# Kernel tuning notes

Hardware: AMD Instinct MI355X
Metric: run time of the kernel (lower is better)

The kernel has to match this reference:

```python
import jax, jax.numpy as jnp
import numpy as np

COMMITMENT_COST = 0.25


def setup_inputs() -> dict:
    key = jax.random.key(0)
    k1, k2 = jax.random.split(key)
    # z_latents: [B, H, W, D] encoder output latents
    z_latents = jax.random.normal(k1, (128, 32, 32, 64), dtype=jnp.float32)
    # embeddings: [D, K] codebook, uniform init like tf.random_uniform_initializer (default [-0.05, 0.05])
    embeddings = jax.random.uniform(k2, (64, 1024), dtype=jnp.float32, minval=-0.05, maxval=0.05)
    return {"z_latents": z_latents, "embeddings": embeddings}


def reference(z_latents, embeddings):
    d, k = embeddings.shape
    flat = z_latents.reshape(-1, d)  # [N, D]
    # squared L2 distances to each codebook entry: [N, K]
    distances = (
        jnp.sum(flat * flat, axis=1, keepdims=True)
        - 2.0 * (flat @ embeddings)
        + jnp.sum(embeddings * embeddings, axis=0, keepdims=True)
    )
    # argmax(-d) == argmin(d) (both take first occurrence on ties)
    encoding_indices = jnp.argmin(distances, axis=1)  # [N]
    # one-hot @ embeddings.T is just a gather of codebook rows
    quantized = jnp.take(embeddings.T, encoding_indices, axis=0).reshape(z_latents.shape)
    commitment_loss = jnp.mean((jax.lax.stop_gradient(quantized) - z_latents) ** 2)
    embedding_loss = jnp.mean((jax.lax.stop_gradient(z_latents) - quantized) ** 2)
    vq_loss = embedding_loss + COMMITMENT_COST * commitment_loss
    # straight-through estimator
    quantized_st = z_latents + jax.lax.stop_gradient(quantized - z_latents)
    return quantized_st, vq_loss
```

## Files before the change

kernel.cpp:

```cpp
#include <hip/hip_runtime.h>

#pragma clang fp contract(off)

typedef __attribute__((ext_vector_type(8))) short short8;
typedef __attribute__((ext_vector_type(4))) float f32x4;

#define MARGIN 0.02f

static __device__ __forceinline__ unsigned short f2b(float f) {
    union { float f; unsigned u; } x; x.f = f;
    unsigned u = x.u;
    return (unsigned short)((u + 0x7FFFu + ((u >> 16) & 1u)) >> 16);
}

template <int ES>
static __device__ __forceinline__ float np_dist(
    const float* __restrict__ zr, const float* __restrict__ ecol,
    float zn, float en) {
    float c = 0.f;
    #pragma unroll
    for (int i = 0; i < 64; ++i) c = fmaf(zr[i], ecol[i * ES], c);
    float t = zn - 2.f * c;
    return t + en;
}

template <bool ET, bool EB>
__global__ __launch_bounds__(256) void vq_prep_all(
    const float* __restrict__ E, float* __restrict__ ws_loss,
    float* __restrict__ enorm, float* __restrict__ Et,
    unsigned* __restrict__ EbW) {
    const int t = blockIdx.x * 256 + threadIdx.x;
    if (ET) {
        Et[t] = E[(t & 63) * 1024 + (t >> 6)];
    }
    if (EB) {
        if (t < 32768) {
            const int st = t >> 12;
            const int r = t & 4095;
            const int col = r >> 5;
            const int w = r & 31;
            const int g = w >> 2;
            const int d0 = ((g ^ (col & 7)) << 3) | ((w & 3) << 1);
            const int gc = st * 128 + col;
            const unsigned lo = f2b(E[d0 * 1024 + gc]);
            const unsigned hi = f2b(E[(d0 + 1) * 1024 + gc]);
            EbW[t] = lo | (hi << 16);
        }
    }
    if (t < 1024) {
        const float* colp = E + t;
        float s2 = 0.f;
        #pragma unroll
        for (int d = 0; d < 64; ++d) {
            float v = colp[d * 1024];
            s2 = fmaf(v, v, s2);
        }
        enorm[t] = s2;
        if (t == 0) *ws_loss = 0.f;
    }
}

template <bool USE_ET, bool USE_EB>
__global__ __launch_bounds__(256) void vq_main(
    const float* __restrict__ z, const float* __restrict__ E,
    const float* __restrict__ Et, const unsigned short* __restrict__ Eb,
    const float* __restrict__ enorm,
    float* __restrict__ ws_loss, float* __restrict__ out) {
    __shared__ unsigned short sB[2][128 * 64];
    __shared__ float sEn[1024];
    __shared__ float sZn[128];
    __shared__ int sIdx[128];
    __shared__ float sRed[4];

    const int tid = threadIdx.x;
    const int w = tid >> 6;
    const int l = tid & 63;
    const int quad = l >> 4;
    const int m = l & 15;
    const int b = blockIdx.x;

    ((float4*)sEn)[tid] = ((const float4*)enorm)[tid];

    if (tid < 128) {
        const float* zr = z + (b * 128 + tid) * 64;
        float S[16];
        #pragma unroll
        for (int u = 0; u < 16; ++u) { float v = zr[u]; S[u] = v * v; }
        #pragma unroll
        for (int t = 1; t < 4; ++t)
            #pragma unroll
            for (int u = 0; u < 16; ++u) {
                float v = zr[16 * t + u];
                float sq = v * v;
                S[u] = S[u] + sq;
            }
        float R0 = (S[0] + S[4]) + (S[8] + S[12]);
        float R1 = (S[1] + S[5]) + (S[9] + S[13]);
        float R2 = (S[2] + S[6]) + (S[10] + S[14]);
        float R3 = (S[3] + S[7]) + (S[11] + S[15]);
        sZn[tid] = (R0 + R1) + (R2 + R3);
    }

    short8 a[2][2];
    #pragma unroll
    for (int rt = 0; rt < 2; ++rt) {
        const int rowl = w * 32 + rt * 16 + m;
        #pragma unroll
        for (int s = 0; s < 2; ++s) {
            const float* zp = z + (b * 128 + rowl) * 64 + s * 32 + quad * 8;
            union { float4 v; float f[4]; } u0, u1;
            u0.v = *(const float4*)zp;
            u1.v = *(const float4*)(zp + 4);
            short8 av;
            #pragma unroll
            for (int j = 0; j < 4; ++j) av[j] = (short)f2b(u0.f[j]);
            #pragma unroll
            for (int j = 0; j < 4; ++j) av[4 + j] = (short)f2b(u1.f[j]);
            a[rt][s] = av;
        }
    }

    float v1p[2][4], v2p[2][4];
    #pragma unroll
    for (int rt = 0; rt < 2; ++rt)
        #pragma unroll
        for (int r = 0; r < 4; ++r) { v1p[rt][r] = 3.4e38f; v2p[rt][r] = 3.4e38f; }

    short8 nx0, nx1, nx2, nx3;
    if (USE_EB) {
        const short8* s0 = (const short8*)Eb;
        short8* dp = (short8*)sB[0];
        #pragma unroll
        for (int i = 0; i < 4; ++i) dp[tid + i * 256] = s0[tid + i * 256];
        __syncthreads();
    }

    for (int st = 0; st < 8; ++st) {
        const unsigned short* sBc;
        if (USE_EB) {
            if (st < 7) {
                const short8* sn = (const short8*)(Eb + (st + 1) * 8192);
                nx0 = sn[tid];
                nx1 = sn[tid + 256];
                nx2 = sn[tid + 512];
                nx3 = sn[tid + 768];
            }
            sBc = sB[st & 1];
        } else {
            #pragma unroll
            for (int i = 0; i < 4; ++i) {
                const int u = tid + i * 256;
                const int d0 = (u & 31) * 2;
                const int cg = u >> 5;
                const float* e0 = E + d0 * 1024 + st * 128 + cg * 4;
                union { float4 v; float f[4]; } va, vb;
                va.v = *(const float4*)e0;
                vb.v = *(const float4*)(e0 + 1024);
                #pragma unroll
                for (int j = 0; j < 4; ++j) {
                    const int col = cg * 4 + j;
                    const unsigned lo = f2b(va.f[j]);
                    const unsigned hi = f2b(vb.f[j]);
                    const int gi = col * 8 + ((d0 >> 3) ^ (col & 7));
                    *(unsigned*)&sB[0][gi * 8 + (d0 & 7)] = lo | (hi << 16);
                }
            }
            __syncthreads();
            sBc = sB[0];
        }

        #pragma unroll
        for (int ct = 0; ct < 8; ++ct) {
            const int c = st * 8 + ct;
            const int colb = (ct * 16 + m) * 8;
            short8 b0 = *(const short8*)&sBc[(colb + (quad ^ (m & 7))) * 8];
            short8 b1 = *(const short8*)&sBc[(colb + ((4 + quad) ^ (m & 7))) * 8];
            f32x4 acc0 = {0.f, 0.f, 0.f, 0.f};
            f32x4 acc1 = {0.f, 0.f, 0.f, 0.f};
            acc0 = __builtin_amdgcn_mfma_f32_16x16x32_bf16(a[0][0], b0, acc0, 0, 0, 0);
            acc0 = __builtin_amdgcn_mfma_f32_16x16x32_bf16(a[0][1], b1, acc0, 0, 0, 0);
            acc1 = __builtin_amdgcn_mfma_f32_16x16x32_bf16(a[1][0], b0, acc1, 0, 0, 0);
            acc1 = __builtin_amdgcn_mfma_f32_16x16x32_bf16(a[1][1], b1, acc1, 0, 0, 0);
            const float en = sEn[c * 16 + m];
            #pragma unroll
            for (int r = 0; r < 4; ++r) {
                float p0 = fmaf(-2.f, acc0[r], en);
                p0 = __uint_as_float((__float_as_uint(p0) & 0xFFFFFFC0u) | (unsigned)c);
                v2p[0][r] = __builtin_amdgcn_fmed3f(p0, v1p[0][r], v2p[0][r]);
                v1p[0][r] = fminf(p0, v1p[0][r]);
                float p1 = fmaf(-2.f, acc1[r], en);
                p1 = __uint_as_float((__float_as_uint(p1) & 0xFFFFFFC0u) | (unsigned)c);
                v2p[1][r] = __builtin_amdgcn_fmed3f(p1, v1p[1][r], v2p[1][r]);
                v1p[1][r] = fminf(p1, v1p[1][r]);
            }
        }

        if (USE_EB) {
            if (st < 7) {
                short8* dn = (short8*)sB[(st & 1) ^ 1];
                dn[tid] = nx0;
                dn[tid + 256] = nx1;
                dn[tid + 512] = nx2;
                dn[tid + 768] = nx3;
            }
            __syncthreads();
        } else {
            __syncthreads();
        }
    }

    float la = 0.f;
    #pragma unroll
    for (int rt = 0; rt < 2; ++rt) {
        #pragma unroll
        for (int r = 0; r < 4; ++r) {
            float pv1 = v1p[rt][r];
            float vb = pv1;
            #pragma unroll
            for (int mask = 1; mask <= 8; mask <<= 1)
                vb = fminf(vb, __shfl_xor(vb, mask));
            const int rowl = w * 32 + rt * 16 + quad * 4 + r;
            const float zn = sZn[rowl];
            const float* zr = z + (b * 128 + rowl) * 64;
            float d = 3.4e38f;
            int kk = 0x7fffffff;
            if (pv1 <= vb + MARGIN) {
                kk = (int)(__float_as_uint(pv1) & 63u) * 16 + m;
                d = USE_ET ? np_dist<1>(zr, Et + kk * 64, zn, sEn[kk])
                           : np_dist<1024>(zr, E + kk, zn, sEn[kk]);
            }
            float pv2 = v2p[rt][r];
            if (pv2 <= vb + MARGIN) {
                int kc = (int)(__float_as_uint(pv2) & 63u) * 16 + m;
                float dd = USE_ET ? np_dist<1>(zr, Et + kc * 64, zn, sEn[kc])
                                  : np_dist<1024>(zr, E + kc, zn, sEn[kc]);
                if (dd < d || (dd == d && kc < kk)) { d = dd; kk = kc; }
            }
            #pragma unroll
            for (int mask = 1; mask <= 8; mask <<= 1) {
                float d2 = __shfl_xor(d, mask);
                int c2 = __shfl_xor(kk, mask);
                bool take = (d2 < d) || (d2 == d && c2 < kk);
                d = take ? d2 : d;
                kk = take ? c2 : kk;
            }
            if (m == 0) {
                sIdx[rowl] = kk;
                la += d;
            }
        }
    }
    __syncthreads();

    {
        const int row_local = w * 32 + (l >> 1);
        const int half = l & 1;
        const int idx = sIdx[row_local];
        union { float s[32]; float4 f[8]; } tmp;
        if (USE_ET) {
            const float4* src = (const float4*)(Et + idx * 64 + half * 32);
            #pragma unroll
            for (int q4 = 0; q4 < 8; ++q4) tmp.f[q4] = src[q4];
        } else {
            #pragma unroll
            for (int dd = 0; dd < 32; ++dd) tmp.s[dd] = E[(half * 32 + dd) * 1024 + idx];
        }
        float4* dst = (float4*)(out + (b * 128 + row_local) * 64 + half * 32);
        #pragma unroll
        for (int q4 = 0; q4 < 8; ++q4) dst[q4] = tmp.f[q4];
    }

    #pragma unroll
    for (int mask = 32; mask >= 1; mask >>= 1) la += __shfl_xor(la, mask);
    if (l == 0) sRed[w] = la;
    __syncthreads();
    if (tid == 0) atomicAdd(ws_loss, sRed[0] + sRed[1] + sRed[2] + sRed[3]);
}

__global__ void vq_final(const float* __restrict__ ws_loss,
                         float* __restrict__ out) {
    out[8388608] = (*ws_loss) * (1.25f / 8388608.f);
}

extern "C" void kernel_launch(void* const* d_in, const int* in_sizes, int n_in,
                              void* d_out, int out_size, void* d_ws, size_t ws_size,
                              hipStream_t stream) {
    const float* z = (const float*)d_in[0];
    const float* E = (const float*)d_in[1];
    float* out = (float*)d_out;

    char* ws = (char*)d_ws;
    float* loss = (float*)ws;
    float* enorm = (float*)(ws + 128);
    unsigned short* Eb = (unsigned short*)(ws + 8192);
    float* Et = (float*)(ws + 139264);
    const bool useEb = ws_size >= (size_t)139264;
    const bool useEt = ws_size >= (size_t)401408;

    if (useEt) {
        vq_prep_all<true, true><<<256, 256, 0, stream>>>(E, loss, enorm, Et, (unsigned*)Eb);
        vq_main<true, true><<<1024, 256, 0, stream>>>(z, E, Et, Eb, enorm, loss, out);
    } else if (useEb) {
        vq_prep_all<false, true><<<256, 256, 0, stream>>>(E, loss, enorm, Et, (unsigned*)Eb);
        vq_main<false, true><<<1024, 256, 0, stream>>>(z, E, Et, Eb, enorm, loss, out);
    } else {
        vq_prep_all<false, false><<<256, 256, 0, stream>>>(E, loss, enorm, Et, (unsigned*)Eb);
        vq_main<false, false><<<1024, 256, 0, stream>>>(z, E, Et, Eb, enorm, loss, out);
    }
    vq_final<<<1, 1, 0, stream>>>(loss, out);
}
```

Baseline: 158.4 us.

## Read MFMA-ready codebook fragments straight from global and fuse loss finalization

The prep kernel now stages a 64-column slab of the codebook in shared memory and writes the bf16 codebook in a per-lane MFMA fragment layout. The main kernel loads B fragments straight from global/L2, dropping the double-buffered LDS staging and its per-stage barriers, which also shrinks LDS use and may allow more resident blocks. The separate finalize launch is replaced by a last-block-done atomic counter that writes the loss. This trades LDS traffic and syncs for repeated L2 reads of the 128KB codebook by every wave.

```diff
diff --git a/kernel.cpp b/kernel.cpp
--- a/kernel.cpp
+++ b/kernel.cpp
@@ -27,37 +27,54 @@
 template <bool ET, bool EB>
 __global__ __launch_bounds__(256) void vq_prep_all(
     const float* __restrict__ E, float* __restrict__ ws_loss,
-    float* __restrict__ enorm, float* __restrict__ Et,
-    unsigned* __restrict__ EbW) {
-    const int t = blockIdx.x * 256 + threadIdx.x;
+    unsigned* __restrict__ ws_cnt, float* __restrict__ enorm,
+    float* __restrict__ Et, unsigned* __restrict__ EbW) {
+    __shared__ float sT[64][65];
+    const int tid = threadIdx.x;
+    const int w = tid >> 6;
+    const int m64 = tid & 63;
+    const int c0 = blockIdx.x * 64;
+
+    #pragma unroll
+    for (int r = 0; r < 16; ++r) {
+        const int row = r * 4 + w;
+        sT[row][m64] = E[row * 1024 + c0 + m64];
+    }
+    __syncthreads();
+
     if (ET) {
-        Et[t] = E[(t & 63) * 1024 + (t >> 6)];
+        #pragma unroll
+        for (int it = 0; it < 16; ++it) {
+            const int e = it * 256 + tid;
+            const int col = e >> 6, d = e & 63;
+            Et[(c0 + col) * 64 + d] = sT[d][col];
+        }
     }
     if (EB) {
-        if (t < 32768) {
-            const int st = t >> 12;
-            const int r = t & 4095;
-            const int col = r >> 5;
-            const int w = r & 31;
-            const int g = w >> 2;
-            const int d0 = ((g ^ (col & 7)) << 3) | ((w & 3) << 1);
-            const int gc = st * 128 + col;
-            const unsigned lo = f2b(E[d0 * 1024 + gc]);
-            const unsigned hi = f2b(E[(d0 + 1) * 1024 + gc]);
-            EbW[t] = lo | (hi << 16);
-        }
-    }
-    if (t < 1024) {
-        const float* colp = E + t;
+        #pragma unroll
+        for (int it = 0; it < 8; ++it) {
+            const int w0 = it * 256 + tid;
+            const int cl = w0 >> 9;
+            const int s = (w0 >> 8) & 1;
+            const int l = (w0 >> 2) & 63;
+            const int j = (w0 & 3) * 2;
+            const int d = s * 32 + (l >> 4) * 8 + j;
+            const int col = cl * 16 + (l & 15);
+            const unsigned lo = f2b(sT[d][col]);
+            const unsigned hi = f2b(sT[d + 1][col]);
+            EbW[(blockIdx.x * 4 + cl) * 512 + (w0 & 511)] = lo | (hi << 16);
+        }
+    }
+    if (tid < 64) {
         float s2 = 0.f;
         #pragma unroll
         for (int d = 0; d < 64; ++d) {
-            float v = colp[d * 1024];
+            float v = sT[d][tid];
             s2 = fmaf(v, v, s2);
         }
-        enorm[t] = s2;
-        if (t == 0) *ws_loss = 0.f;
-    }
+        enorm[c0 + tid] = s2;
+    }
+    if (blockIdx.x == 0 && tid == 0) { *ws_loss = 0.f; *ws_cnt = 0u; }
 }
 
 template <bool USE_ET, bool USE_EB>
@@ -65,8 +82,9 @@
     const float* __restrict__ z, const float* __restrict__ E,
     const float* __restrict__ Et, const unsigned short* __restrict__ Eb,
     const float* __restrict__ enorm,
-    float* __restrict__ ws_loss, float* __restrict__ out) {
-    __shared__ unsigned short sB[2][128 * 64];
+    float* __restrict__ ws_loss, unsigned* __restrict__ ws_cnt,
+    float* __restrict__ out) {
+    __shared__ unsigned short sB[USE_EB ? 64 : 128 * 64];
     __shared__ float sEn[1024];
     __shared__ float sZn[128];
     __shared__ int sIdx[128];
@@ -126,27 +144,34 @@
         #pragma unroll
         for (int r = 0; r < 4; ++r) { v1p[rt][r] = 3.4e38f; v2p[rt][r] = 3.4e38f; }
 
-    short8 nx0, nx1, nx2, nx3;
-    if (USE_EB) {
-        const short8* s0 = (const short8*)Eb;
-        short8* dp = (short8*)sB[0];
-        #pragma unroll
-        for (int i = 0; i < 4; ++i) dp[tid + i * 256] = s0[tid + i * 256];
+    if constexpr (USE_EB) {
         __syncthreads();
-    }
-
-    for (int st = 0; st < 8; ++st) {
-        const unsigned short* sBc;
-        if (USE_EB) {
-            if (st < 7) {
-                const short8* sn = (const short8*)(Eb + (st + 1) * 8192);
-                nx0 = sn[tid];
-                nx1 = sn[tid + 256];
-                nx2 = sn[tid + 512];
-                nx3 = sn[tid + 768];
-            }
-            sBc = sB[st & 1];
-        } else {
+        const unsigned short* __restrict__ ebp = Eb + l * 8;
+        #pragma unroll 8
+        for (int c = 0; c < 64; ++c) {
+            short8 b0 = *(const short8*)(ebp + c * 1024);
+            short8 b1 = *(const short8*)(ebp + c * 1024 + 512);
+            f32x4 acc0 = {0.f, 0.f, 0.f, 0.f};
+            f32x4 acc1 = {0.f, 0.f, 0.f, 0.f};
+            acc0 = __builtin_amdgcn_mfma_f32_16x16x32_bf16(a[0][0], b0, acc0, 0, 0, 0);
+            acc0 = __builtin_amdgcn_mfma_f32_16x16x32_bf16(a[0][1], b1, acc0, 0, 0, 0);
+            acc1 = __builtin_amdgcn_mfma_f32_16x16x32_bf16(a[1][0], b0, acc1, 0, 0, 0);
+            acc1 = __builtin_amdgcn_mfma_f32_16x16x32_bf16(a[1][1], b1, acc1, 0, 0, 0);
+            const float en = sEn[c * 16 + m];
+            #pragma unroll
+            for (int r = 0; r < 4; ++r) {
+                float p0 = fmaf(-2.f, acc0[r], en);
+                p0 = __uint_as_float((__float_as_uint(p0) & 0xFFFFFFC0u) | (unsigned)c);
+                v2p[0][r] = __builtin_amdgcn_fmed3f(p0, v1p[0][r], v2p[0][r]);
+                v1p[0][r] = fminf(p0, v1p[0][r]);
+                float p1 = fmaf(-2.f, acc1[r], en);
+                p1 = __uint_as_float((__float_as_uint(p1) & 0xFFFFFFC0u) | (unsigned)c);
+                v2p[1][r] = __builtin_amdgcn_fmed3f(p1, v1p[1][r], v2p[1][r]);
+                v1p[1][r] = fminf(p1, v1p[1][r]);
+            }
+        }
+    } else {
+        for (int st = 0; st < 8; ++st) {
             #pragma unroll
             for (int i = 0; i < 4; ++i) {
                 const int u = tid + i * 256;
@@ -162,49 +187,35 @@
                     const unsigned lo = f2b(va.f[j]);
                     const unsigned hi = f2b(vb.f[j]);
                     const int gi = col * 8 + ((d0 >> 3) ^ (col & 7));
-                    *(unsigned*)&sB[0][gi * 8 + (d0 & 7)] = lo | (hi << 16);
+                    *(unsigned*)&sB[gi * 8 + (d0 & 7)] = lo | (hi << 16);
                 }
             }
             __syncthreads();
-            sBc = sB[0];
-        }
-
-        #pragma unroll
-        for (int ct = 0; ct < 8; ++ct) {
-            const int c = st * 8 + ct;
-            const int colb = (ct * 16 + m) * 8;
-            short8 b0 = *(const short8*)&sBc[(colb + (quad ^ (m & 7))) * 8];
-            short8 b1 = *(const short8*)&sBc[(colb + ((4 + quad) ^ (m & 7))) * 8];
-            f32x4 acc0 = {0.f, 0.f, 0.f, 0.f};
-            f32x4 acc1 = {0.f, 0.f, 0.f, 0.f};
-            acc0 = __builtin_amdgcn_mfma_f32_16x16x32_bf16(a[0][0], b0, acc0, 0, 0, 0);
-            acc0 = __builtin_amdgcn_mfma_f32_16x16x32_bf16(a[0][1], b1, acc0, 0, 0, 0);
-            acc1 = __builtin_amdgcn_mfma_f32_16x16x32_bf16(a[1][0], b0, acc1, 0, 0, 0);
-            acc1 = __builtin_amdgcn_mfma_f32_16x16x32_bf16(a[1][1], b1, acc1, 0, 0, 0);
-            const float en = sEn[c * 16 + m];
-            #pragma unroll
-            for (int r = 0; r < 4; ++r) {
-                float p0 = fmaf(-2.f, acc0[r], en);
-                p0 = __uint_as_float((__float_as_uint(p0) & 0xFFFFFFC0u) | (unsigned)c);
-                v2p[0][r] = __builtin_amdgcn_fmed3f(p0, v1p[0][r], v2p[0][r]);
-                v1p[0][r] = fminf(p0, v1p[0][r]);
-                float p1 = fmaf(-2.f, acc1[r], en);
-                p1 = __uint_as_float((__float_as_uint(p1) & 0xFFFFFFC0u) | (unsigned)c);
-                v2p[1][r] = __builtin_amdgcn_fmed3f(p1, v1p[1][r], v2p[1][r]);
-                v1p[1][r] = fminf(p1, v1p[1][r]);
-            }
-        }
-
-        if (USE_EB) {
-            if (st < 7) {
-                short8* dn = (short8*)sB[(st & 1) ^ 1];
-                dn[tid] = nx0;
-                dn[tid + 256] = nx1;
-                dn[tid + 512] = nx2;
-                dn[tid + 768] = nx3;
-            }
-            __syncthreads();
-        } else {
+            #pragma unroll
+            for (int ct = 0; ct < 8; ++ct) {
+                const int c = st * 8 + ct;
+                const int colb = (ct * 16 + m) * 8;
+                short8 b0 = *(const short8*)&sB[(colb + (quad ^ (m & 7))) * 8];
+                short8 b1 = *(const short8*)&sB[(colb + ((4 + quad) ^ (m & 7))) * 8];
+                f32x4 acc0 = {0.f, 0.f, 0.f, 0.f};
+                f32x4 acc1 = {0.f, 0.f, 0.f, 0.f};
+                acc0 = __builtin_amdgcn_mfma_f32_16x16x32_bf16(a[0][0], b0, acc0, 0, 0, 0);
+                acc0 = __builtin_amdgcn_mfma_f32_16x16x32_bf16(a[0][1], b1, acc0, 0, 0, 0);
+                acc1 = __builtin_amdgcn_mfma_f32_16x16x32_bf16(a[1][0], b0, acc1, 0, 0, 0);
+                acc1 = __builtin_amdgcn_mfma_f32_16x16x32_bf16(a[1][1], b1, acc1, 0, 0, 0);
+                const float en = sEn[c * 16 + m];
+                #pragma unroll
+                for (int r = 0; r < 4; ++r) {
+                    float p0 = fmaf(-2.f, acc0[r], en);
+                    p0 = __uint_as_float((__float_as_uint(p0) & 0xFFFFFFC0u) | (unsigned)c);
+                    v2p[0][r] = __builtin_amdgcn_fmed3f(p0, v1p[0][r], v2p[0][r]);
+                    v1p[0][r] = fminf(p0, v1p[0][r]);
+                    float p1 = fmaf(-2.f, acc1[r], en);
+                    p1 = __uint_as_float((__float_as_uint(p1) & 0xFFFFFFC0u) | (unsigned)c);
+                    v2p[1][r] = __builtin_amdgcn_fmed3f(p1, v1p[1][r], v2p[1][r]);
+                    v1p[1][r] = fminf(p1, v1p[1][r]);
+                }
+            }
             __syncthreads();
         }
     }
@@ -274,12 +285,16 @@
     for (int mask = 32; mask >= 1; mask >>= 1) la += __shfl_xor(la, mask);
     if (l == 0) sRed[w] = la;
     __syncthreads();
-    if (tid == 0) atomicAdd(ws_loss, sRed[0] + sRed[1] + sRed[2] + sRed[3]);
-}
-
-__global__ void vq_final(const float* __restrict__ ws_loss,
-                         float* __restrict__ out) {
-    out[8388608] = (*ws_loss) * (1.25f / 8388608.f);
+
+    if (tid == 0) {
+        atomicAdd(ws_loss, sRed[0] + sRed[1] + sRed[2] + sRed[3]);
+        __threadfence();
+        const unsigned done = atomicAdd(ws_cnt, 1u);
+        if (done == 1023u) {
+            const float total = atomicAdd(ws_loss, 0.f);
+            out[8388608] = total * (1.25f / 8388608.f);
+        }
+    }
 }
 
 extern "C" void kernel_launch(void* const* d_in, const int* in_sizes, int n_in,
@@ -291,6 +306,7 @@
 
     char* ws = (char*)d_ws;
     float* loss = (float*)ws;
+    unsigned* cnt = (unsigned*)(ws + 4);
     float* enorm = (float*)(ws + 128);
     unsigned short* Eb = (unsigned short*)(ws + 8192);
     float* Et = (float*)(ws + 139264);
@@ -298,14 +314,13 @@
     const bool useEt = ws_size >= (size_t)401408;
 
     if (useEt) {
-        vq_prep_all<true, true><<<256, 256, 0, stream>>>(E, loss, enorm, Et, (unsigned*)Eb);
-        vq_main<true, true><<<1024, 256, 0, stream>>>(z, E, Et, Eb, enorm, loss, out);
+        vq_prep_all<true, true><<<16, 256, 0, stream>>>(E, loss, cnt, enorm, Et, (unsigned*)Eb);
+        vq_main<true, true><<<1024, 256, 0, stream>>>(z, E, Et, Eb, enorm, loss, cnt, out);
     } else if (useEb) {
-        vq_prep_all<false, true><<<256, 256, 0, stream>>>(E, loss, enorm, Et, (unsigned*)Eb);
-        vq_main<false, true><<<1024, 256, 0, stream>>>(z, E, Et, Eb, enorm, loss, out);
+        vq_prep_all<false, true><<<16, 256, 0, stream>>>(E, loss, cnt, enorm, Et, (unsigned*)Eb);
+        vq_main<false, true><<<1024, 256, 0, stream>>>(z, E, Et, Eb, enorm, loss, cnt, out);
     } else {
-        vq_prep_all<false, false><<<256, 256, 0, stream>>>(E, loss, enorm, Et, (unsigned*)Eb);
-        vq_main<false, false><<<1024, 256, 0, stream>>>(z, E, Et, Eb, enorm, loss, out);
-    }
-    vq_final<<<1, 1, 0, stream>>>(loss, out);
-}
+        vq_prep_all<false, false><<<16, 256, 0, stream>>>(E, loss, cnt, enorm, Et, (unsigned*)Eb);
+        vq_main<false, false><<<1024, 256, 0, stream>>>(z, E, Et, Eb, enorm, loss, cnt, out);
+    }
+}
```

New measurement: 197.6 us. 1.25x slower.
